# Kernel optimization log

Hardware: AMD Instinct MI355X
Metric: run time of the kernel (lower is better)

Reference implementation:

```python
import jax, jax.numpy as jnp
import numpy as np

B, D, P = 2048, 768, 200
DOWN = [(384, 768), (192, 384), (96, 192), (48, 96)]
UP = [(96, 48), (192, 96), (384, 192), (768, 384)]


def setup_inputs() -> dict:
    key = jax.random.key(0)
    ks = jax.random.split(key, 32)
    inp = {
        "x": jax.random.normal(ks[0], (B, D), jnp.float32),
        "aW": jax.random.normal(ks[1], (D, D), jnp.float32) * 0.02,
        "ab": jax.random.normal(ks[2], (D,), jnp.float32) * 0.02,
        "protos": jax.random.normal(ks[3], (P, D), jnp.float32),
    }
    k = 4
    for i, (o, ii) in enumerate(DOWN):
        inp[f"Wd{i}"] = jax.random.normal(ks[k], (o, ii), jnp.float32) * (1.0 / np.sqrt(ii)); k += 1
        inp[f"bd{i}"] = jax.random.normal(ks[k], (o,), jnp.float32) * 0.02; k += 1
    for i, (o, ii) in enumerate(UP):
        inp[f"Wu{i}"] = jax.random.normal(ks[k], (o, ii), jnp.float32) * (1.0 / np.sqrt(ii)); k += 1
        inp[f"bu{i}"] = jax.random.normal(ks[k], (o,), jnp.float32) * 0.02; k += 1
    return inp


def _adopter_net(x, Wds, bds, Wus, bus):
    # down path with skip storage
    x_inter = []
    h = x
    for Wd, bd in zip(Wds, bds):
        h = jax.nn.relu(h @ Wd.T + bd)
        x_inter.append(h)
    # up path: residual adds for middle layers (i==1 uses x_inter[-2], i==2 uses x_inter[-3])
    n = len(Wus)
    for i, (Wu, bu) in enumerate(zip(Wus, bus)):
        if i == 0 or i == n - 1:
            h = jax.nn.relu(h @ Wu.T + bu)
        else:
            h = jax.nn.relu((h + x_inter[-i - 1]) @ Wu.T + bu)
    return h


def reference(x, aW, ab, Wd0, bd0, Wd1, bd1, Wd2, bd2, Wd3, bd3,
              Wu0, bu0, Wu1, bu1, Wu2, bu2, Wu3, bu3, protos):
    Wds, bds = [Wd0, Wd1, Wd2, Wd3], [bd0, bd1, bd2, bd3]
    Wus, bus = [Wu0, Wu1, Wu2, Wu3], [bu0, bu1, bu2, bu3]
    # features = x + adapter(x) + adopters(x)
    features = x + (x @ aW.T + ab) + _adopter_net(x, Wds, bds, Wus, bus)  # [B, D]
    # fused per-prototype negative L1 distance (replaces Python loop over PrototypeBase)
    logits = -jnp.sum(jnp.abs(features[:, None, :] - protos[None, :, :]), axis=-1)  # [B, P]
    return logits
```

## Files before the change

kernel.cpp:

```cpp
#include <hip/hip_runtime.h>

typedef __attribute__((ext_vector_type(8))) __bf16 bf16x8;
typedef __attribute__((ext_vector_type(4))) float f32x4;
typedef _Float16 hf2 __attribute__((ext_vector_type(2)));
typedef _Float16 hf8 __attribute__((ext_vector_type(8)));
typedef unsigned short u16;
typedef struct { hf2 v[4]; } hf2x4;

__device__ __forceinline__ float bf2f(u16 h) {
    return __uint_as_float(((unsigned int)h) << 16);
}
__device__ __forceinline__ u16 f2bf(float f) {
    unsigned int u = __float_as_uint(f);
    u += 0x7fffu + ((u >> 16) & 1u);
    return (u16)(u >> 16);
}

#if __has_builtin(__builtin_amdgcn_fdot2)
__device__ __forceinline__ float FDOT2(hf2 a, hf2 b, float c) {
    return __builtin_amdgcn_fdot2(a, b, c, false);
}
#else
__device__ __forceinline__ float FDOT2(hf2 a, hf2 b, float c) {
    return c + (float)a[0] + (float)a[1];
}
#endif

#define GLOAD_LDS16(gsrc, ldst)                                                          \
    __builtin_amdgcn_global_load_lds(                                                    \
        (__attribute__((address_space(1))) unsigned int*)(gsrc),                         \
        (__attribute__((address_space(3))) unsigned int*)(ldst), 16, 0, 0)

struct CvtDesc { const float* src; u16* dst; int N, K, Npad, Kpad, blk0, fmt; };
struct CvtTab { CvtDesc t[11]; };

__device__ __forceinline__ void do_cvt(const CvtTab& tab, int vb, int tid) {
    int ti = 0;
#pragma unroll
    for (int j = 1; j < 11; ++j)
        if (vb >= tab.t[j].blk0) ti = j;
    const CvtDesc c = tab.t[ti];
    long i = (long)(vb - c.blk0) * 256 + tid;
    long tot = (long)c.Npad * c.Kpad;
    if (i >= tot) return;
    int n = (int)(i / c.Kpad);
    int k = (int)(i - (long)n * c.Kpad);
    float v = (n < c.N && k < c.K) ? c.src[(long)n * c.K + k] : 0.f;
    c.dst[i] = c.fmt ? __builtin_bit_cast(u16, (_Float16)v) : f2bf(v);
}

__global__ __launch_bounds__(256) void cvt_k(CvtTab tab) {
    do_cvt(tab, blockIdx.x, threadIdx.x);
}

template<int RELU, int HASRES, int RESF16, int MODE>
__device__ __forceinline__ void gemm128_body(
    char* lds,
    const u16* __restrict__ A, int lda,
    const u16* __restrict__ W, int ldw,
    const float* __restrict__ bias,
    u16* __restrict__ outB, int ldo,
    const void* __restrict__ res, int ldr,
    _Float16* __restrict__ outH,
    int nk, int mb, int nb)
{
    const int tid = threadIdx.x;
    const int wave = tid >> 6, lane = tid & 63;
    const int lr = lane & 15, lk = lane >> 4;
    const int wr = wave >> 1, wc = wave & 1;

    f32x4 acc[4][2];
#pragma unroll
    for (int i = 0; i < 4; ++i)
#pragma unroll
        for (int j = 0; j < 2; ++j)
#pragma unroll
            for (int e = 0; e < 4; ++e) acc[i][j][e] = 0.f;

    int ra[4], la[4], rb_[2], lb[2];
#pragma unroll
    for (int t = 0; t < 4; ++t) {
        int g = t * 256 + tid;
        ra[t] = g >> 3; la[t] = (g & 7) ^ (ra[t] & 7);
    }
#pragma unroll
    for (int t = 0; t < 2; ++t) {
        int g = t * 256 + tid;
        rb_[t] = g >> 3; lb[t] = (g & 7) ^ (rb_[t] & 7);
    }

    auto STAGE = [&](int b, int kt) {
        const int kk = kt * 64;
        char* dA = lds + b * 24576;
        char* dB = dA + 16384;
#pragma unroll
        for (int t = 0; t < 4; ++t)
            GLOAD_LDS16(A + (size_t)(mb + ra[t]) * lda + kk + la[t] * 8,
                        dA + t * 4096 + wave * 1024);
#pragma unroll
        for (int t = 0; t < 2; ++t)
            GLOAD_LDS16(W + (size_t)(nb + rb_[t]) * ldw + kk + lb[t] * 8,
                        dB + t * 4096 + wave * 1024);
    };
    auto COMPUTE = [&](int b) {
        char* sA = lds + b * 24576;
        char* sB = sA + 16384;
#pragma unroll
        for (int ks = 0; ks < 2; ++ks) {
            bf16x8 af[4], bfr[2];
#pragma unroll
            for (int mi = 0; mi < 4; ++mi) {
                int m_loc = wr * 64 + mi * 16 + lr;
                int gr = (ks * 4 + lk) ^ (m_loc & 7);
                af[mi] = *(const bf16x8*)(sA + m_loc * 128 + gr * 16);
            }
#pragma unroll
            for (int ni = 0; ni < 2; ++ni) {
                int n_loc = wc * 32 + ni * 16 + lr;
                int gr = (ks * 4 + lk) ^ (n_loc & 7);
                bfr[ni] = *(const bf16x8*)(sB + n_loc * 128 + gr * 16);
            }
#pragma unroll
            for (int mi = 0; mi < 4; ++mi)
#pragma unroll
                for (int ni = 0; ni < 2; ++ni)
                    acc[mi][ni] = __builtin_amdgcn_mfma_f32_16x16x32_bf16(
                        af[mi], bfr[ni], acc[mi][ni], 0, 0, 0);
        }
    };

    STAGE(0, 0);
    __syncthreads();
    int b = 0;
    for (int kt = 0; kt < nk - 1; ++kt) {
        STAGE(b ^ 1, kt + 1);
        COMPUTE(b);
        __syncthreads();
        b ^= 1;
    }
    COMPUTE(b);

#pragma unroll
    for (int mi = 0; mi < 4; ++mi) {
#pragma unroll
        for (int ni = 0; ni < 2; ++ni) {
            const int n_g = nb + wc * 32 + ni * 16 + lr;
            const float bv = bias[n_g];
#pragma unroll
            for (int r = 0; r < 4; ++r) {
                const int m_g = mb + wr * 64 + mi * 16 + lk * 4 + r;
                float v = acc[mi][ni][r] + bv;
                if (RELU) v = fmaxf(v, 0.f);
                if (HASRES) {
                    if (RESF16)
                        v += (float)((const _Float16*)res)[(size_t)m_g * ldr + n_g];
                    else
                        v += bf2f(((const u16*)res)[(size_t)m_g * ldr + n_g]);
                }
                if (MODE == 2) outH[(size_t)m_g * 768 + n_g] = (_Float16)v;
                else           outB[(size_t)m_g * ldo + n_g] = f2bf(v);
            }
        }
    }
}

__global__ __launch_bounds__(256, 2) void gemm_d0_cvt(
    const u16* __restrict__ xb, const u16* __restrict__ Wd0b,
    const float* __restrict__ bd0, u16* __restrict__ h1, CvtTab tabB)
{
    __shared__ __align__(16) char lds[49152];
    const int bid = blockIdx.x;
    if (bid < 96) {
        gemm128_body<1, 0, 0, 0>(lds, xb, 768, Wd0b, 768, bd0, h1, 384,
                                 nullptr, 0, nullptr, 12,
                                 (bid & 15) * 128, (bid >> 4) * 64);
    } else {
        do_cvt(tabB, bid - 96, threadIdx.x);
    }
}

template<int K, int NPAD, int NREAL, int RES, int OUTG>
__device__ __forceinline__ void layer16(
    const u16* __restrict__ W, int ldw, const float* __restrict__ bias,
    const u16* actIn, int ldin,
    u16* actOut, int ldout,
    const u16* resid, int ldres,
    u16* __restrict__ gout, int ldg)
{
    constexpr int TPW = NPAD / 64;
    const int tid = threadIdx.x;
    const int wave = tid >> 6, lane = tid & 63;
    const int lr = lane & 15, lk = lane >> 4;

    f32x4 acc[TPW];
#pragma unroll
    for (int t = 0; t < TPW; ++t)
#pragma unroll
        for (int e = 0; e < 4; ++e) acc[t][e] = 0.f;

#pragma unroll
    for (int kk = 0; kk < K / 32; ++kk) {
        const bf16x8 a = *(const bf16x8*)&actIn[lr * ldin + kk * 32 + lk * 8];
#pragma unroll
        for (int t = 0; t < TPW; ++t) {
            const int nc = (wave * TPW + t) * 16 + lr;
            const bf16x8 b = *(const bf16x8*)&W[(size_t)nc * ldw + kk * 32 + lk * 8];
            acc[t] = __builtin_amdgcn_mfma_f32_16x16x32_bf16(a, b, acc[t], 0, 0, 0);
        }
    }
#pragma unroll
    for (int t = 0; t < TPW; ++t) {
        const int nc = (wave * TPW + t) * 16 + lr;
        const float bv = (nc < NREAL) ? bias[nc] : 0.f;
#pragma unroll
        for (int r = 0; r < 4; ++r) {
            const int row = lk * 4 + r;
            float v = fmaxf(acc[t][r] + bv, 0.f);
            if (RES) v += bf2f(resid[row * ldres + nc]);
            const u16 o = f2bf(v);
            if (OUTG) gout[(size_t)row * ldg + nc] = o;
            else      actOut[row * ldout + nc] = o;
        }
    }
}

__global__ __launch_bounds__(256, 2) void chain_ad(
    const u16* __restrict__ xb,
    const u16* __restrict__ aWb, const float* __restrict__ ab,
    _Float16* __restrict__ featH,
    const u16* __restrict__ h1,
    const u16* __restrict__ Wd1b, const float* __restrict__ bd1,
    const u16* __restrict__ Wd2b, const float* __restrict__ bd2,
    const u16* __restrict__ Wd3b, const float* __restrict__ bd3,
    const u16* __restrict__ Wu0b, const float* __restrict__ bu0,
    const u16* __restrict__ Wu1b, const float* __restrict__ bu1,
    const u16* __restrict__ Wu2b, const float* __restrict__ bu2,
    u16* __restrict__ u2)
{
    __shared__ __align__(16) char smem[49152];
    const int bid = blockIdx.x;
    const int tid = threadIdx.x;

    if (bid < 192) {
        gemm128_body<0, 1, 0, 2>(smem, xb, 768, aWb, 768, ab, nullptr, 0,
                                 xb, 768, featH, 12,
                                 (bid & 15) * 128, (bid >> 4) * 64);
        return;
    }
    u16* As = (u16*)smem;
    u16* Bs = (u16*)(smem + 12544);
    u16* Cs = (u16*)(smem + 18944);
    u16* Ds = (u16*)(smem + 23296);
    const int rb = (bid - 192) * 16;

    for (int i = tid; i < 768; i += 256) {
        const int r = i / 48, c = i - r * 48;
        *(bf16x8*)&As[r * 392 + c * 8] =
            *(const bf16x8*)&h1[(size_t)(rb + r) * 384 + c * 8];
    }
    __syncthreads();
    layer16<384, 192, 192, 0, 0>(Wd1b, 384, bd1, As, 392, Bs, 200, nullptr, 0, nullptr, 0);
    __syncthreads();
    layer16<192, 128,  96, 0, 0>(Wd2b, 192, bd2, Bs, 200, Cs, 136, nullptr, 0, nullptr, 0);
    __syncthreads();
    layer16<128,  64,  48, 0, 0>(Wd3b, 128, bd3, Cs, 136, Ds,  72, nullptr, 0, nullptr, 0);
    __syncthreads();
    u16* E = As;
    u16* F = As + 16 * 136;
    layer16< 64, 128,  96, 1, 0>(Wu0b,  64, bu0, Ds,  72, E, 136, Cs, 136, nullptr, 0);
    __syncthreads();
    layer16<128, 192, 192, 1, 0>(Wu1b, 128, bu1, E, 136, F, 200, Bs, 200, nullptr, 0);
    __syncthreads();
    layer16<192, 384, 384, 0, 1>(Wu2b, 192, bu2, F, 200, nullptr, 0, nullptr, 0,
                                 u2 + (size_t)rb * 384, 384);
}

__global__ __launch_bounds__(256, 2) void gemm_u3add(
    const u16* __restrict__ u2, const u16* __restrict__ Wu3b,
    const float* __restrict__ bu3, _Float16* __restrict__ featH)
{
    __shared__ __align__(16) char lds[49152];
    gemm128_body<1, 1, 1, 2>(lds, u2, 384, Wu3b, 384, bu3, nullptr, 0,
                             featH, 768, featH, 6,
                             blockIdx.x * 128, blockIdx.y * 64);
}

__global__ __launch_bounds__(256) void l1_kernel(
    const _Float16* __restrict__ feat, const _Float16* __restrict__ protos,
    float* __restrict__ part)
{
    __shared__ _Float16 fs[128][96];
    __shared__ hf2 pt[48][64];
    const int tid = threadIdx.x;
    const int tp = tid & 15, tr = tid >> 4;
    const int rb = blockIdx.x * 128;
    const int pb = blockIdx.y * 64;
    const int db = blockIdx.z * 96;

    for (int i = tid; i < 1536; i += 256) {
        const int r = i / 12, c = i - r * 12;
        *(hf8*)&fs[r][c * 8] =
            *(const hf8*)&feat[(size_t)(rb + r) * 768 + db + c * 8];
    }
    {
        const int sp = tid & 63, q = tid >> 6;
#pragma unroll
        for (int t = 0; t < 3; ++t) {
            const hf8 v = *(const hf8*)&protos[(size_t)(pb + sp) * 768 + db + q * 24 + t * 8];
            const hf2x4 w = __builtin_bit_cast(hf2x4, v);
            const int p0 = q * 12 + t * 4;
#pragma unroll
            for (int e = 0; e < 4; ++e)
                pt[p0 + e][sp] = w.v[e];
        }
    }
    __syncthreads();

    float acc[8][4];
#pragma unroll
    for (int i = 0; i < 8; ++i)
#pragma unroll
        for (int j = 0; j < 4; ++j) acc[i][j] = 0.f;

    const hf2 one2 = {(_Float16)1.0f, (_Float16)1.0f};
#pragma unroll 2
    for (int g = 0; g < 12; ++g) {
        hf2x4 F2[8];
#pragma unroll
        for (int i = 0; i < 8; ++i)
            F2[i] = __builtin_bit_cast(hf2x4, *(const hf8*)&fs[tr + 16 * i][g * 8]);
        hf2x4 P2[4];
#pragma unroll
        for (int q = 0; q < 4; ++q)
            P2[q] = __builtin_bit_cast(hf2x4, *(const hf8*)&pt[g * 4 + q][tp * 4]);
#pragma unroll
        for (int q = 0; q < 4; ++q) {
#pragma unroll
            for (int j = 0; j < 4; ++j) {
                const hf2 pj = P2[q].v[j];
#pragma unroll
                for (int i = 0; i < 8; ++i) {
                    hf2 d = F2[i].v[q] - pj;
                    unsigned ud = __builtin_bit_cast(unsigned, d) & 0x7FFF7FFFu;
                    acc[i][j] = FDOT2(__builtin_bit_cast(hf2, ud), one2, acc[i][j]);
                }
            }
        }
    }
    const int p = pb + tp * 4;
    if (p < 200) {
#pragma unroll
        for (int i = 0; i < 8; ++i) {
            float4 v = {-acc[i][0], -acc[i][1], -acc[i][2], -acc[i][3]};
            *(float4*)&part[((size_t)(rb + tr + 16 * i) * 8 + blockIdx.z) * 200 + p] = v;
        }
    }
}

__global__ __launch_bounds__(256) void l1_reduce(
    const float* __restrict__ part, float* __restrict__ out)
{
    const int row = blockIdx.x;
    const int p = threadIdx.x;
    if (p < 200) {
        float s = 0.f;
#pragma unroll
        for (int z = 0; z < 8; ++z)
            s += part[((size_t)row * 8 + z) * 200 + p];
        out[(size_t)row * 200 + p] = s;
    }
}

static constexpr size_t OFF_PART  = 0;
static constexpr size_t OFF_XB    = 0;
static constexpr size_t OFF_AWB   = 3145728;
static constexpr size_t OFF_WD0   = 4325376;
static constexpr size_t OFF_WD1   = 4915200;
static constexpr size_t OFF_WD2   = 5062656;
static constexpr size_t OFF_WD3   = 5111808;
static constexpr size_t OFF_WU0   = 5128192;
static constexpr size_t OFF_WU1   = 5144576;
static constexpr size_t OFF_WU2   = 5193728;
static constexpr size_t OFF_WU3   = 5341184;
static constexpr size_t OFF_H1    = 5931008;
static constexpr size_t OFF_U2    = 10387456;
static constexpr size_t OFF_FEATH = 19660800;
static constexpr size_t OFF_PROH  = 22806528;

extern "C" void kernel_launch(void* const* d_in, const int* in_sizes, int n_in,
                              void* d_out, int out_size, void* d_ws, size_t ws_size,
                              hipStream_t stream) {
    const float* x      = (const float*)d_in[0];
    const float* aW     = (const float*)d_in[1];
    const float* ab     = (const float*)d_in[2];
    const float* protos = (const float*)d_in[3];
    const float* Wd[4]  = {(const float*)d_in[4], (const float*)d_in[6],
                           (const float*)d_in[8], (const float*)d_in[10]};
    const float* bd[4]  = {(const float*)d_in[5], (const float*)d_in[7],
                           (const float*)d_in[9], (const float*)d_in[11]};
    const float* Wu[4]  = {(const float*)d_in[12], (const float*)d_in[14],
                           (const float*)d_in[16], (const float*)d_in[18]};
    const float* bu[4]  = {(const float*)d_in[13], (const float*)d_in[15],
                           (const float*)d_in[17], (const float*)d_in[19]};
    float* out = (float*)d_out;
    char* ws = (char*)d_ws;

    u16* xb    = (u16*)(ws + OFF_XB);
    u16* aWb   = (u16*)(ws + OFF_AWB);
    u16* Wd0b  = (u16*)(ws + OFF_WD0);
    u16* Wd1b  = (u16*)(ws + OFF_WD1);
    u16* Wd2b  = (u16*)(ws + OFF_WD2);
    u16* Wd3b  = (u16*)(ws + OFF_WD3);
    u16* Wu0b  = (u16*)(ws + OFF_WU0);
    u16* Wu1b  = (u16*)(ws + OFF_WU1);
    u16* Wu2b  = (u16*)(ws + OFF_WU2);
    u16* Wu3b  = (u16*)(ws + OFF_WU3);
    u16* h1    = (u16*)(ws + OFF_H1);
    u16* u2    = (u16*)(ws + OFF_U2);
    float* part = (float*)(ws + OFF_PART);
    _Float16* featH = (_Float16*)(ws + OFF_FEATH);
    _Float16* proH  = (_Float16*)(ws + OFF_PROH);

    const int SENT = 0x7FFFFFFF;

    CvtTab tabA;
    int blkA = 0;
    tabA.t[0] = {x,     xb,   2048, 768, 2048, 768, 0, 0};
    blkA += 2048 * 768 / 256;
    tabA.t[1] = {Wd[0], Wd0b, 384,  768, 384,  768, blkA, 0};
    blkA += 384 * 768 / 256;
    for (int j = 2; j < 11; ++j) tabA.t[j].blk0 = SENT;
    cvt_k<<<blkA, 256, 0, stream>>>(tabA);

    CvtTab tabB;
    int blkB = 0;
    auto setB = [&](int i, const float* s, u16* d, int N, int K, int Np, int Kp,
                    int fmt) {
        tabB.t[i] = {s, d, N, K, Np, Kp, blkB, fmt};
        blkB += (Np * Kp + 255) / 256;
    };
    setB(0, aW,     aWb,        768, 768, 768, 768, 0);
    setB(1, Wd[1],  Wd1b,       192, 384, 192, 384, 0);
    setB(2, Wd[2],  Wd2b,       96,  192, 128, 192, 0);
    setB(3, Wd[3],  Wd3b,       48,  96,  64,  128, 0);
    setB(4, Wu[0],  Wu0b,       96,  48,  128, 64,  0);
    setB(5, Wu[1],  Wu1b,       192, 96,  192, 128, 0);
    setB(6, Wu[2],  Wu2b,       384, 192, 384, 192, 0);
    setB(7, Wu[3],  Wu3b,       768, 384, 768, 384, 0);
    setB(8, protos, (u16*)proH, 200, 768, 256, 768, 1);
    for (int j = 9; j < 11; ++j) tabB.t[j].blk0 = SENT;
    gemm_d0_cvt<<<96 + blkB, 256, 0, stream>>>(xb, Wd0b, bd[0], h1, tabB);

    chain_ad<<<320, 256, 0, stream>>>(xb, aWb, ab, featH, h1,
        Wd1b, bd[1], Wd2b, bd[2], Wd3b, bd[3],
        Wu0b, bu[0], Wu1b, bu[1], Wu2b, bu[2], u2);

    gemm_u3add<<<dim3(16, 12), 256, 0, stream>>>(u2, Wu3b, bu[3], featH);

    l1_kernel<<<dim3(16, 4, 8), 256, 0, stream>>>(featH, proH, part);
    l1_reduce<<<dim3(2048), 256, 0, stream>>>(part, out);
}
```

Before: 79.08 us.

## Move adapter GEMM into first kernel and split-K the chain across 512 threads

The adapter GEMM (x·aWᵀ + x) moves out of the chain kernel into the first GEMM launch, and aW's bf16 conversion moves into the initial convert kernel. The layer chain becomes a dedicated 512-thread kernel where each layer is split in K across two wave groups, with partial sums combined through LDS. The goal is to halve the serial per-layer MFMA latency of the small-row chain and to overlap the adapter GEMM with the d0 GEMM. The cost is an extra LDS round-trip and barrier per layer, plus a larger first kernel that now waits on a bigger convert pass.

```diff
diff --git a/kernel.cpp b/kernel.cpp
--- a/kernel.cpp
+++ b/kernel.cpp
@@ -164,9 +164,11 @@
     }
 }
 
-__global__ __launch_bounds__(256, 2) void gemm_d0_cvt(
+__global__ __launch_bounds__(256, 2) void gemm_d0ad_cvt(
     const u16* __restrict__ xb, const u16* __restrict__ Wd0b,
-    const float* __restrict__ bd0, u16* __restrict__ h1, CvtTab tabB)
+    const float* __restrict__ bd0, u16* __restrict__ h1,
+    const u16* __restrict__ aWb, const float* __restrict__ ab,
+    _Float16* __restrict__ featH, CvtTab tabB)
 {
     __shared__ __align__(16) char lds[49152];
     const int bid = blockIdx.x;
@@ -174,22 +176,31 @@
         gemm128_body<1, 0, 0, 0>(lds, xb, 768, Wd0b, 768, bd0, h1, 384,
                                  nullptr, 0, nullptr, 12,
                                  (bid & 15) * 128, (bid >> 4) * 64);
+    } else if (bid < 288) {
+        const int b2 = bid - 96;
+        gemm128_body<0, 1, 0, 2>(lds, xb, 768, aWb, 768, ab, nullptr, 0,
+                                 xb, 768, featH, 12,
+                                 (b2 & 15) * 128, (b2 >> 4) * 64);
     } else {
-        do_cvt(tabB, bid - 96, threadIdx.x);
+        do_cvt(tabB, bid - 288, threadIdx.x);
     }
 }
 
 template<int K, int NPAD, int NREAL, int RES, int OUTG>
-__device__ __forceinline__ void layer16(
+__device__ __forceinline__ void layer16s(
     const u16* __restrict__ W, int ldw, const float* __restrict__ bias,
     const u16* actIn, int ldin,
     u16* actOut, int ldout,
     const u16* resid, int ldres,
-    u16* __restrict__ gout, int ldg)
+    u16* __restrict__ gout, int ldg,
+    float* comb)
 {
     constexpr int TPW = NPAD / 64;
+    constexpr int KK = K / 32;
+    constexpr int KH = KK / 2;
     const int tid = threadIdx.x;
-    const int wave = tid >> 6, lane = tid & 63;
+    const int w = tid >> 6, lane = tid & 63;
+    const int nw = w & 3, kw = w >> 2;
     const int lr = lane & 15, lk = lane >> 4;
 
     f32x4 acc[TPW];
@@ -199,35 +210,43 @@
         for (int e = 0; e < 4; ++e) acc[t][e] = 0.f;
 
 #pragma unroll
-    for (int kk = 0; kk < K / 32; ++kk) {
+    for (int s = 0; s < KH; ++s) {
+        const int kk = kw * KH + s;
         const bf16x8 a = *(const bf16x8*)&actIn[lr * ldin + kk * 32 + lk * 8];
 #pragma unroll
         for (int t = 0; t < TPW; ++t) {
-            const int nc = (wave * TPW + t) * 16 + lr;
+            const int nc = (nw * TPW + t) * 16 + lr;
             const bf16x8 b = *(const bf16x8*)&W[(size_t)nc * ldw + kk * 32 + lk * 8];
             acc[t] = __builtin_amdgcn_mfma_f32_16x16x32_bf16(a, b, acc[t], 0, 0, 0);
         }
     }
-#pragma unroll
-    for (int t = 0; t < TPW; ++t) {
-        const int nc = (wave * TPW + t) * 16 + lr;
-        const float bv = (nc < NREAL) ? bias[nc] : 0.f;
-#pragma unroll
-        for (int r = 0; r < 4; ++r) {
-            const int row = lk * 4 + r;
-            float v = fmaxf(acc[t][r] + bv, 0.f);
-            if (RES) v += bf2f(resid[row * ldres + nc]);
-            const u16 o = f2bf(v);
-            if (OUTG) gout[(size_t)row * ldg + nc] = o;
-            else      actOut[row * ldout + nc] = o;
-        }
-    }
-}
-
-__global__ __launch_bounds__(256, 2) void chain_ad(
-    const u16* __restrict__ xb,
-    const u16* __restrict__ aWb, const float* __restrict__ ab,
-    _Float16* __restrict__ featH,
+    if (kw == 1) {
+#pragma unroll
+        for (int t = 0; t < TPW; ++t)
+            *(f32x4*)(comb + ((size_t)(nw * TPW + t) * 64 + lane) * 4) = acc[t];
+    }
+    __syncthreads();
+    if (kw == 0) {
+#pragma unroll
+        for (int t = 0; t < TPW; ++t) {
+            const f32x4 o = *(const f32x4*)(comb + ((size_t)(nw * TPW + t) * 64 + lane) * 4);
+            const int nc = (nw * TPW + t) * 16 + lr;
+            const float bv = (nc < NREAL) ? bias[nc] : 0.f;
+#pragma unroll
+            for (int r = 0; r < 4; ++r) {
+                const int row = lk * 4 + r;
+                float v = fmaxf(acc[t][r] + o[r] + bv, 0.f);
+                if (RES) v += bf2f(resid[row * ldres + nc]);
+                const u16 ov = f2bf(v);
+                if (OUTG) gout[(size_t)row * ldg + nc] = ov;
+                else      actOut[row * ldout + nc] = ov;
+            }
+        }
+    }
+    __syncthreads();
+}
+
+__global__ __launch_bounds__(512) void chain512(
     const u16* __restrict__ h1,
     const u16* __restrict__ Wd1b, const float* __restrict__ bd1,
     const u16* __restrict__ Wd2b, const float* __restrict__ bd2,
@@ -237,42 +256,29 @@
     const u16* __restrict__ Wu2b, const float* __restrict__ bu2,
     u16* __restrict__ u2)
 {
-    __shared__ __align__(16) char smem[49152];
-    const int bid = blockIdx.x;
+    __shared__ u16 As[16 * 392];
+    __shared__ u16 Bs[16 * 200];
+    __shared__ u16 Cs[16 * 136];
+    __shared__ u16 Ds[16 * 72];
+    __shared__ float comb[6144];
     const int tid = threadIdx.x;
-
-    if (bid < 192) {
-        gemm128_body<0, 1, 0, 2>(smem, xb, 768, aWb, 768, ab, nullptr, 0,
-                                 xb, 768, featH, 12,
-                                 (bid & 15) * 128, (bid >> 4) * 64);
-        return;
-    }
-    u16* As = (u16*)smem;
-    u16* Bs = (u16*)(smem + 12544);
-    u16* Cs = (u16*)(smem + 18944);
-    u16* Ds = (u16*)(smem + 23296);
-    const int rb = (bid - 192) * 16;
-
-    for (int i = tid; i < 768; i += 256) {
+    const int rb = blockIdx.x * 16;
+
+    for (int i = tid; i < 768; i += 512) {
         const int r = i / 48, c = i - r * 48;
         *(bf16x8*)&As[r * 392 + c * 8] =
             *(const bf16x8*)&h1[(size_t)(rb + r) * 384 + c * 8];
     }
     __syncthreads();
-    layer16<384, 192, 192, 0, 0>(Wd1b, 384, bd1, As, 392, Bs, 200, nullptr, 0, nullptr, 0);
-    __syncthreads();
-    layer16<192, 128,  96, 0, 0>(Wd2b, 192, bd2, Bs, 200, Cs, 136, nullptr, 0, nullptr, 0);
-    __syncthreads();
-    layer16<128,  64,  48, 0, 0>(Wd3b, 128, bd3, Cs, 136, Ds,  72, nullptr, 0, nullptr, 0);
-    __syncthreads();
+    layer16s<384, 192, 192, 0, 0>(Wd1b, 384, bd1, As, 392, Bs, 200, nullptr, 0, nullptr, 0, comb);
+    layer16s<192, 128,  96, 0, 0>(Wd2b, 192, bd2, Bs, 200, Cs, 136, nullptr, 0, nullptr, 0, comb);
+    layer16s<128,  64,  48, 0, 0>(Wd3b, 128, bd3, Cs, 136, Ds,  72, nullptr, 0, nullptr, 0, comb);
     u16* E = As;
     u16* F = As + 16 * 136;
-    layer16< 64, 128,  96, 1, 0>(Wu0b,  64, bu0, Ds,  72, E, 136, Cs, 136, nullptr, 0);
-    __syncthreads();
-    layer16<128, 192, 192, 1, 0>(Wu1b, 128, bu1, E, 136, F, 200, Bs, 200, nullptr, 0);
-    __syncthreads();
-    layer16<192, 384, 384, 0, 1>(Wu2b, 192, bu2, F, 200, nullptr, 0, nullptr, 0,
-                                 u2 + (size_t)rb * 384, 384);
+    layer16s< 64, 128,  96, 1, 0>(Wu0b,  64, bu0, Ds,  72, E, 136, Cs, 136, nullptr, 0, comb);
+    layer16s<128, 192, 192, 1, 0>(Wu1b, 128, bu1, E, 136, F, 200, Bs, 200, nullptr, 0, comb);
+    layer16s<192, 384, 384, 0, 1>(Wu2b, 192, bu2, F, 200, nullptr, 0, nullptr, 0,
+                                  u2 + (size_t)rb * 384, 384, comb);
 }
 
 __global__ __launch_bounds__(256, 2) void gemm_u3add(
@@ -429,7 +435,9 @@
     blkA += 2048 * 768 / 256;
     tabA.t[1] = {Wd[0], Wd0b, 384,  768, 384,  768, blkA, 0};
     blkA += 384 * 768 / 256;
-    for (int j = 2; j < 11; ++j) tabA.t[j].blk0 = SENT;
+    tabA.t[2] = {aW,    aWb,  768,  768, 768,  768, blkA, 0};
+    blkA += 768 * 768 / 256;
+    for (int j = 3; j < 11; ++j) tabA.t[j].blk0 = SENT;
     cvt_k<<<blkA, 256, 0, stream>>>(tabA);
 
     CvtTab tabB;
@@ -439,19 +447,19 @@
         tabB.t[i] = {s, d, N, K, Np, Kp, blkB, fmt};
         blkB += (Np * Kp + 255) / 256;
     };
-    setB(0, aW,     aWb,        768, 768, 768, 768, 0);
-    setB(1, Wd[1],  Wd1b,       192, 384, 192, 384, 0);
-    setB(2, Wd[2],  Wd2b,       96,  192, 128, 192, 0);
-    setB(3, Wd[3],  Wd3b,       48,  96,  64,  128, 0);
-    setB(4, Wu[0],  Wu0b,       96,  48,  128, 64,  0);
-    setB(5, Wu[1],  Wu1b,       192, 96,  192, 128, 0);
-    setB(6, Wu[2],  Wu2b,       384, 192, 384, 192, 0);
-    setB(7, Wu[3],  Wu3b,       768, 384, 768, 384, 0);
-    setB(8, protos, (u16*)proH, 200, 768, 256, 768, 1);
-    for (int j = 9; j < 11; ++j) tabB.t[j].blk0 = SENT;
-    gemm_d0_cvt<<<96 + blkB, 256, 0, stream>>>(xb, Wd0b, bd[0], h1, tabB);
-
-    chain_ad<<<320, 256, 0, stream>>>(xb, aWb, ab, featH, h1,
+    setB(0, Wd[1],  Wd1b,       192, 384, 192, 384, 0);
+    setB(1, Wd[2],  Wd2b,       96,  192, 128, 192, 0);
+    setB(2, Wd[3],  Wd3b,       48,  96,  64,  128, 0);
+    setB(3, Wu[0],  Wu0b,       96,  48,  128, 64,  0);
+    setB(4, Wu[1],  Wu1b,       192, 96,  192, 128, 0);
+    setB(5, Wu[2],  Wu2b,       384, 192, 384, 192, 0);
+    setB(6, Wu[3],  Wu3b,       768, 384, 768, 384, 0);
+    setB(7, protos, (u16*)proH, 200, 768, 256, 768, 1);
+    for (int j = 8; j < 11; ++j) tabB.t[j].blk0 = SENT;
+    gemm_d0ad_cvt<<<288 + blkB, 256, 0, stream>>>(xb, Wd0b, bd[0], h1,
+                                                  aWb, ab, featH, tabB);
+
+    chain512<<<128, 512, 0, stream>>>(h1,
         Wd1b, bd[1], Wd2b, bd[2], Wd3b, bd[3],
         Wu0b, bu[0], Wu1b, bu[1], Wu2b, bu[2], u2);
 
```

Result: no change. 78.42 us (-0.8%).
